# Optimization experiments

Hardware: AMD Instinct MI355X
Metric: run time of the kernel (lower is better)

The kernel has to match this reference:

```python
import jax, jax.numpy as jnp
import numpy as np

TEMPERATURE = 0.07
MASK_VALUE = -10000.0
EPS = 1e-12  # matches F.normalize eps


def setup_inputs() -> dict:
    key = jax.random.key(0)
    k1, k2 = jax.random.split(key)
    B, D = 8192, 512
    embeddings = jax.random.normal(k1, (B, D), dtype=jnp.float32)
    positive_mask = jax.random.randint(k2, (B, B), 0, 2).astype(bool)
    return {"embeddings": embeddings, "positive_mask": positive_mask}


def reference(embeddings, positive_mask):
    B = embeddings.shape[0]
    # L2 normalize rows (F.normalize with eps clamp)
    norm = jnp.maximum(jnp.linalg.norm(embeddings, axis=1, keepdims=True), EPS)
    e = embeddings / norm
    sim = jnp.matmul(e, e.T) / TEMPERATURE  # (B, B)
    eye = jnp.eye(B, dtype=bool)
    sim = jnp.where(eye, MASK_VALUE, sim)
    pos = positive_mask & ~eye
    counts = pos.sum(axis=1)  # (B,)
    pos_sum = jnp.sum(jnp.where(pos, sim, 0.0), axis=1)  # (B,)
    lse = jax.nn.logsumexp(sim, axis=1)  # (B,)
    pos_mean = pos_sum / jnp.maximum(counts, 1).astype(sim.dtype)
    # rows with positives: -mean(pos) + lse; rows without: just lse
    row_loss = jnp.where(counts > 0, lse - pos_mean, lse)
    return jnp.mean(row_loss)
```

## Files before the change

kernel.cpp:

```cpp
#include <hip/hip_runtime.h>
#include <hip/hip_bf16.h>

#define BN_ 8192
#define DK_ 512
#define TEMP_INV 14.2857142857142857f
#define LOG2E_ 1.44269504088896f
#define MAXOFF 15.0f

typedef __bf16 bf16x8 __attribute__((ext_vector_type(8)));
typedef float f32x4 __attribute__((ext_vector_type(4)));

__device__ inline unsigned short f2bf(float f) {
    unsigned u = __float_as_uint(f);
    return (unsigned short)((u + 0x7FFFu + ((u >> 16) & 1u)) >> 16);
}

__global__ __launch_bounds__(256) void norm_kernel(const float* __restrict__ emb,
                                                   unsigned short* __restrict__ ebf) {
    const int row  = blockIdx.x * 4 + (threadIdx.x >> 6);
    const int lane = threadIdx.x & 63;
    const float4* src = reinterpret_cast<const float4*>(emb + (size_t)row * DK_);
    float4 v0 = src[lane];
    float4 v1 = src[lane + 64];
    float ss = v0.x*v0.x + v0.y*v0.y + v0.z*v0.z + v0.w*v0.w
             + v1.x*v1.x + v1.y*v1.y + v1.z*v1.z + v1.w*v1.w;
#pragma unroll
    for (int off = 1; off < 64; off <<= 1) ss += __shfl_xor(ss, off, 64);
    const float scale = 1.0f / fmaxf(sqrtf(ss), 1e-12f);
    uint2 o0, o1;
    o0.x = (unsigned)f2bf(v0.x * scale) | ((unsigned)f2bf(v0.y * scale) << 16);
    o0.y = (unsigned)f2bf(v0.z * scale) | ((unsigned)f2bf(v0.w * scale) << 16);
    o1.x = (unsigned)f2bf(v1.x * scale) | ((unsigned)f2bf(v1.y * scale) << 16);
    o1.y = (unsigned)f2bf(v1.z * scale) | ((unsigned)f2bf(v1.w * scale) << 16);
    uint2* dst = reinterpret_cast<uint2*>(ebf + (size_t)row * DK_);
    dst[lane]      = o0;
    dst[lane + 64] = o1;
}

__global__ __launch_bounds__(256) void infonce_main(
    const unsigned short* __restrict__ ebf,
    const int* __restrict__ mask,
    float* __restrict__ se, float* __restrict__ ps, float* __restrict__ ct) {

    __shared__ unsigned short As[128 * 64];
    __shared__ unsigned short Bs[128 * 64];
    __shared__ unsigned char  pmB[128 * 16];
    __shared__ float red2[2][128];

    const int t    = threadIdx.x;
    const int lane = t & 63;
    const int wid  = t >> 6;
    const int wr   = wid >> 1;
    const int wc   = wid & 1;
    const int rb   = blockIdx.x;
    const int cb   = blockIdx.y;

    if (t < 128) { red2[0][t] = 0.f; red2[1][t] = 0.f; }

    f32x4 acc[4][4] = {};

    const int sr = t >> 3;
    const int sc = (t & 7) * 8;
    const size_t arow0 = (size_t)(rb * 128 + sr) * DK_ + sc;
    const size_t brow0 = (size_t)(cb * 128 + sr) * DK_ + sc;

    const int mr = t >> 4;
    const int mc = t & 15;
    const int* mbase = mask + (size_t)(rb * 128 + mr) * BN_ + cb * 128 + mc * 8;

    const int r16 = lane & 15;
    const int kg  = (lane >> 4) * 8;

#pragma unroll
    for (int kt = 0; kt < 8; ++kt) {
        const int k0 = kt * 64;
#pragma unroll
        for (int s = 0; s < 4; ++s) {
            __builtin_amdgcn_global_load_lds(
                (const __attribute__((address_space(1))) void*)(ebf + arow0 + (size_t)s * 32 * DK_ + k0),
                (__attribute__((address_space(3))) void*)(As + s * 2048 + t * 8),
                16, 0, 0);
        }
#pragma unroll
        for (int s = 0; s < 4; ++s) {
            __builtin_amdgcn_global_load_lds(
                (const __attribute__((address_space(1))) void*)(ebf + brow0 + (size_t)s * 32 * DK_ + k0),
                (__attribute__((address_space(3))) void*)(Bs + s * 2048 + t * 8),
                16, 0, 0);
        }
        const int4* mp = reinterpret_cast<const int4*>(mbase + (size_t)kt * 16 * BN_);
        const int4 mv0 = mp[0];
        const int4 mv1 = mp[1];

        __syncthreads();

        {
            unsigned by = (unsigned)(mv0.x != 0)        | ((unsigned)(mv0.y != 0) << 1)
                        | ((unsigned)(mv0.z != 0) << 2) | ((unsigned)(mv0.w != 0) << 3)
                        | ((unsigned)(mv1.x != 0) << 4) | ((unsigned)(mv1.y != 0) << 5)
                        | ((unsigned)(mv1.z != 0) << 6) | ((unsigned)(mv1.w != 0) << 7);
            pmB[(kt * 16 + mr) * 16 + mc] = (unsigned char)by;
        }

#pragma unroll
        for (int ks = 0; ks < 2; ++ks) {
            bf16x8 af[4], bfr[4];
#pragma unroll
            for (int fm = 0; fm < 4; ++fm)
                af[fm] = *reinterpret_cast<const bf16x8*>(As + (wr * 64 + fm * 16 + r16) * 64 + ks * 32 + kg);
#pragma unroll
            for (int fn = 0; fn < 4; ++fn)
                bfr[fn] = *reinterpret_cast<const bf16x8*>(Bs + (wc * 64 + fn * 16 + r16) * 64 + ks * 32 + kg);
#pragma unroll
            for (int fm = 0; fm < 4; ++fm)
#pragma unroll
                for (int fn = 0; fn < 4; ++fn)
                    acc[fm][fn] = __builtin_amdgcn_mfma_f32_16x16x32_bf16(bfr[fn], af[fm], acc[fm][fn], 0, 0, 0);
        }
        __syncthreads();
    }

    const float C1 = TEMP_INV * LOG2E_;
    const float C2 = -MAXOFF * LOG2E_;
    const bool  db  = (rb == cb);
    const int   gq4 = (lane >> 4) * 4;

#pragma unroll
    for (int fm = 0; fm < 4; ++fm) {
        const int li = wr * 64 + fm * 16 + (lane & 15);
        const uint4 rv = *reinterpret_cast<const uint4*>(pmB + li * 16);
        const unsigned w0 = wc ? rv.z : rv.x;
        const unsigned w1 = wc ? rv.w : rv.y;
        float lsep = 0.f, posp = 0.f;
#pragma unroll
        for (int fn = 0; fn < 4; ++fn) {
            const unsigned wsel = (fn < 2) ? w0 : w1;
#pragma unroll
            for (int rg = 0; rg < 4; ++rg) {
                const float a = acc[fm][fn][rg];
                const bool dg = db && (wr == wc) && (fm == fn) && ((lane & 15) == gq4 + rg);
                const float ex = dg ? 0.0f : exp2f(fmaf(a, C1, C2));
                lsep += ex;
                const bool p = (((wsel >> ((fn & 1) * 16 + gq4 + rg)) & 1u) != 0u) && !dg;
                posp += p ? a : 0.0f;
            }
        }
        lsep += __shfl_xor(lsep, 16, 64); lsep += __shfl_xor(lsep, 32, 64);
        posp += __shfl_xor(posp, 16, 64); posp += __shfl_xor(posp, 32, 64);
        if ((lane >> 4) == 0) {
            atomicAdd(&red2[0][li], lsep);
            atomicAdd(&red2[1][li], posp * TEMP_INV);
        }
    }
    __syncthreads();
    if (t < 128) {
        const uint4 rv = *reinterpret_cast<const uint4*>(pmB + t * 16);
        float cnt = (float)(__popc(rv.x) + __popc(rv.y) + __popc(rv.z) + __popc(rv.w));
        if (db) {
            const unsigned wsel = (t < 64) ? ((t < 32) ? rv.x : rv.y)
                                           : ((t < 96) ? rv.z : rv.w);
            cnt -= (float)((wsel >> (t & 31)) & 1u);
        }
        const int i = rb * 128 + t;
        atomicAdd(&se[i], red2[0][t]);
        atomicAdd(&ps[i], red2[1][t]);
        atomicAdd(&ct[i], cnt);
    }
}

__global__ __launch_bounds__(256) void finalize_kernel(const float* __restrict__ se,
                                                       const float* __restrict__ ps,
                                                       const float* __restrict__ ct,
                                                       float* __restrict__ out) {
    __shared__ float red[256];
    const int t = threadIdx.x;
    const int i = blockIdx.x * 256 + t;
    const float lse = logf(se[i]) + MAXOFF;
    red[t] = lse - ps[i] / fmaxf(ct[i], 1.0f);
    __syncthreads();
    for (int s = 128; s > 0; s >>= 1) {
        if (t < s) red[t] += red[t + s];
        __syncthreads();
    }
    if (t == 0) atomicAdd(out, red[0] * (1.0f / (float)BN_));
}

extern "C" void kernel_launch(void* const* d_in, const int* in_sizes, int n_in,
                              void* d_out, int out_size, void* d_ws, size_t ws_size,
                              hipStream_t stream) {
    const float* emb  = (const float*)d_in[0];
    const int*   mask = (const int*)d_in[1];
    float* out = (float*)d_out;

    char* ws = (char*)d_ws;
    unsigned short* ebf = (unsigned short*)ws;
    float* se = (float*)(ws + (size_t)8 * 1024 * 1024);
    float* ps = se + BN_;
    float* ct = ps + BN_;

    hipMemsetAsync(se, 0, (size_t)3 * BN_ * sizeof(float), stream);
    hipMemsetAsync(out, 0, sizeof(float), stream);
    norm_kernel<<<BN_ / 4, 256, 0, stream>>>(emb, ebf);
    infonce_main<<<dim3(64, 64), 256, 0, stream>>>(ebf, mask, se, ps, ct);
    finalize_kernel<<<BN_ / 256, 256, 0, stream>>>(se, ps, ct, out);
}
```

Before: 133.6 us.

## Exploit similarity symmetry by computing only upper-triangular tiles

Launches only the 2080 upper-triangular 128x128 tiles of the similarity matrix and maps a linear block id to (rb, cb). Each off-diagonal tile loads both its mask tile and the transposed mask tile. It then accumulates the row-wise and column-wise exp sums and positive sums, halving the GEMM and exp work. The cost is a heavier epilogue with extra shuffles and shared atomics, uneven per-block work, and more global atomics per block.

```diff
diff --git a/kernel.cpp b/kernel.cpp
--- a/kernel.cpp
+++ b/kernel.cpp
@@ -44,18 +44,26 @@
 
     __shared__ unsigned short As[128 * 64];
     __shared__ unsigned short Bs[128 * 64];
-    __shared__ unsigned char  pmB[128 * 16];
-    __shared__ float red2[2][128];
+    __shared__ unsigned char  pmB [128 * 16];
+    __shared__ unsigned char  pmBT[128 * 16];
+    __shared__ float redR[2][128];
+    __shared__ float redC[2][128];
 
     const int t    = threadIdx.x;
     const int lane = t & 63;
     const int wid  = t >> 6;
     const int wr   = wid >> 1;
     const int wc   = wid & 1;
-    const int rb   = blockIdx.x;
-    const int cb   = blockIdx.y;
-
-    if (t < 128) { red2[0][t] = 0.f; red2[1][t] = 0.f; }
+
+    const int bid = blockIdx.x;
+    int rb = (int)((129.0f - sqrtf(16641.0f - 8.0f * (float)bid)) * 0.5f);
+    while (64 * (rb + 1) - ((rb + 1) * rb) / 2 <= bid) ++rb;
+    while (64 * rb - (rb * (rb - 1)) / 2 > bid) --rb;
+    const int cb = rb + (bid - (64 * rb - (rb * (rb - 1)) / 2));
+    const bool offd = (rb != cb);
+    const bool db   = !offd;
+
+    if (t < 128) { redR[0][t] = 0.f; redR[1][t] = 0.f; redC[0][t] = 0.f; redC[1][t] = 0.f; }
 
     f32x4 acc[4][4] = {};
 
@@ -66,7 +74,8 @@
 
     const int mr = t >> 4;
     const int mc = t & 15;
-    const int* mbase = mask + (size_t)(rb * 128 + mr) * BN_ + cb * 128 + mc * 8;
+    const int* mbase  = mask + (size_t)(rb * 128 + mr) * BN_ + cb * 128 + mc * 8;
+    const int* mbaseT = mask + (size_t)(cb * 128 + mr) * BN_ + rb * 128 + mc * 8;
 
     const int r16 = lane & 15;
     const int kg  = (lane >> 4) * 8;
@@ -91,6 +100,12 @@
         const int4* mp = reinterpret_cast<const int4*>(mbase + (size_t)kt * 16 * BN_);
         const int4 mv0 = mp[0];
         const int4 mv1 = mp[1];
+        int4 tw0, tw1;
+        if (offd) {
+            const int4* tp = reinterpret_cast<const int4*>(mbaseT + (size_t)kt * 16 * BN_);
+            tw0 = tp[0];
+            tw1 = tp[1];
+        }
 
         __syncthreads();
 
@@ -100,6 +115,13 @@
                         | ((unsigned)(mv1.x != 0) << 4) | ((unsigned)(mv1.y != 0) << 5)
                         | ((unsigned)(mv1.z != 0) << 6) | ((unsigned)(mv1.w != 0) << 7);
             pmB[(kt * 16 + mr) * 16 + mc] = (unsigned char)by;
+            if (offd) {
+                unsigned byT = (unsigned)(tw0.x != 0)        | ((unsigned)(tw0.y != 0) << 1)
+                             | ((unsigned)(tw0.z != 0) << 2) | ((unsigned)(tw0.w != 0) << 3)
+                             | ((unsigned)(tw1.x != 0) << 4) | ((unsigned)(tw1.y != 0) << 5)
+                             | ((unsigned)(tw1.z != 0) << 6) | ((unsigned)(tw1.w != 0) << 7);
+                pmBT[(kt * 16 + mr) * 16 + mc] = (unsigned char)byT;
+            }
         }
 
 #pragma unroll
@@ -122,34 +144,65 @@
 
     const float C1 = TEMP_INV * LOG2E_;
     const float C2 = -MAXOFF * LOG2E_;
-    const bool  db  = (rb == cb);
-    const int   gq4 = (lane >> 4) * 4;
-
+    const int l15 = lane & 15;
+    const int g   = lane >> 4;
+    const int gq4 = g * 4;
+
+    uint2 rw[4];
 #pragma unroll
     for (int fm = 0; fm < 4; ++fm) {
-        const int li = wr * 64 + fm * 16 + (lane & 15);
-        const uint4 rv = *reinterpret_cast<const uint4*>(pmB + li * 16);
-        const unsigned w0 = wc ? rv.z : rv.x;
-        const unsigned w1 = wc ? rv.w : rv.y;
-        float lsep = 0.f, posp = 0.f;
-#pragma unroll
-        for (int fn = 0; fn < 4; ++fn) {
-            const unsigned wsel = (fn < 2) ? w0 : w1;
-#pragma unroll
-            for (int rg = 0; rg < 4; ++rg) {
+        const uint4 rv = *reinterpret_cast<const uint4*>(pmB + (wr * 64 + fm * 16 + l15) * 16);
+        rw[fm].x = wc ? rv.z : rv.x;
+        rw[fm].y = wc ? rv.w : rv.y;
+    }
+    float lseA[4] = {0.f, 0.f, 0.f, 0.f};
+    float posA[4] = {0.f, 0.f, 0.f, 0.f};
+
+#pragma unroll
+    for (int fn = 0; fn < 4; ++fn) {
+#pragma unroll
+        for (int rg = 0; rg < 4; ++rg) {
+            const int jl = wc * 64 + fn * 16 + gq4 + rg;
+            uint2 tv;
+            if (offd) tv = *reinterpret_cast<const uint2*>(pmBT + jl * 16 + wr * 8);
+            float colL = 0.f, colP = 0.f;
+#pragma unroll
+            for (int fm = 0; fm < 4; ++fm) {
                 const float a = acc[fm][fn][rg];
-                const bool dg = db && (wr == wc) && (fm == fn) && ((lane & 15) == gq4 + rg);
+                const bool dg = db && (wr == wc) && (fm == fn) && (l15 == gq4 + rg);
                 const float ex = dg ? 0.0f : exp2f(fmaf(a, C1, C2));
-                lsep += ex;
+                lseA[fm] += ex;
+                const unsigned wsel = (fn < 2) ? rw[fm].x : rw[fm].y;
                 const bool p = (((wsel >> ((fn & 1) * 16 + gq4 + rg)) & 1u) != 0u) && !dg;
-                posp += p ? a : 0.0f;
+                posA[fm] += p ? a : 0.0f;
+                if (offd) {
+                    colL += ex;
+                    const unsigned cw = (fm < 2) ? tv.x : tv.y;
+                    colP += ((cw >> ((fm & 1) * 16 + l15)) & 1u) ? a : 0.0f;
+                }
             }
-        }
-        lsep += __shfl_xor(lsep, 16, 64); lsep += __shfl_xor(lsep, 32, 64);
-        posp += __shfl_xor(posp, 16, 64); posp += __shfl_xor(posp, 32, 64);
-        if ((lane >> 4) == 0) {
-            atomicAdd(&red2[0][li], lsep);
-            atomicAdd(&red2[1][li], posp * TEMP_INV);
+            if (offd) {
+#pragma unroll
+                for (int off = 1; off < 16; off <<= 1) {
+                    colL += __shfl_xor(colL, off, 64);
+                    colP += __shfl_xor(colP, off, 64);
+                }
+                if (l15 == 0) {
+                    atomicAdd(&redC[0][jl], colL);
+                    atomicAdd(&redC[1][jl], colP * TEMP_INV);
+                }
+            }
+        }
+    }
+#pragma unroll
+    for (int fm = 0; fm < 4; ++fm) {
+        float L = lseA[fm], P = posA[fm];
+        L += __shfl_xor(L, 16, 64); L += __shfl_xor(L, 32, 64);
+        P += __shfl_xor(P, 16, 64); P += __shfl_xor(P, 32, 64);
+        if (g == 0) {
+            const int li = wr * 64 + fm * 16 + l15;
+            atomicAdd(&redR[0][li], L);
+            atomicAdd(&redR[1][li], P * TEMP_INV);
         }
     }
     __syncthreads();
@@ -162,9 +215,17 @@
             cnt -= (float)((wsel >> (t & 31)) & 1u);
         }
         const int i = rb * 128 + t;
-        atomicAdd(&se[i], red2[0][t]);
-        atomicAdd(&ps[i], red2[1][t]);
+        atomicAdd(&se[i], redR[0][t]);
+        atomicAdd(&ps[i], redR[1][t]);
         atomicAdd(&ct[i], cnt);
+    } else if (offd) {
+        const int r = t - 128;
+        const uint4 tvr = *reinterpret_cast<const uint4*>(pmBT + r * 16);
+        const float cnt = (float)(__popc(tvr.x) + __popc(tvr.y) + __popc(tvr.z) + __popc(tvr.w));
+        const int j = cb * 128 + r;
+        atomicAdd(&se[j], redC[0][r]);
+        atomicAdd(&ps[j], redC[1][r]);
+        atomicAdd(&ct[j], cnt);
     }
 }
 
@@ -201,6 +262,6 @@
     hipMemsetAsync(se, 0, (size_t)3 * BN_ * sizeof(float), stream);
     hipMemsetAsync(out, 0, sizeof(float), stream);
     norm_kernel<<<BN_ / 4, 256, 0, stream>>>(emb, ebf);
-    infonce_main<<<dim3(64, 64), 256, 0, stream>>>(ebf, mask, se, ps, ct);
+    infonce_main<<<2080, 256, 0, stream>>>(ebf, mask, se, ps, ct);
     finalize_kernel<<<BN_ / 256, 256, 0, stream>>>(se, ps, ct, out);
 }
```

Result: slower. 224.6 us (+68.1%).

## Double-buffer LDS tiles and prefetch mask rows two stages ahead

Applied to the files above, without the earlier changes.

The main GEMM kernel now keeps two LDS buffers for the A and B tiles. It issues the global-to-LDS loads for the next k-step before computing the current one, and loads mask values two k-steps ahead into registers. Explicit vmcnt waits and one barrier per iteration replace the two __syncthreads, so memory latency can overlap the MFMA work. In exchange it doubles the tile LDS footprint, adds a launch bound of 2 blocks per CU that may constrain registers, and relies on hand-counted vmcnt values for correctness.

```diff
diff --git a/kernel.cpp b/kernel.cpp
--- a/kernel.cpp
+++ b/kernel.cpp
@@ -37,13 +37,13 @@
     dst[lane + 64] = o1;
 }
 
-__global__ __launch_bounds__(256) void infonce_main(
+__global__ __launch_bounds__(256, 2) void infonce_main(
     const unsigned short* __restrict__ ebf,
     const int* __restrict__ mask,
     float* __restrict__ se, float* __restrict__ ps, float* __restrict__ ct) {
 
-    __shared__ unsigned short As[128 * 64];
-    __shared__ unsigned short Bs[128 * 64];
+    __shared__ unsigned short As[2][128 * 64];
+    __shared__ unsigned short Bs[2][128 * 64];
     __shared__ unsigned char  pmB[128 * 16];
     __shared__ float red2[2][128];
 
@@ -71,54 +71,81 @@
     const int r16 = lane & 15;
     const int kg  = (lane >> 4) * 8;
 
+#define STAGE(buf, kt)                                                                     \
+    {                                                                                      \
+        const int k0_ = (kt) * 64;                                                         \
+        _Pragma("unroll")                                                                  \
+        for (int s = 0; s < 4; ++s) {                                                      \
+            __builtin_amdgcn_global_load_lds(                                              \
+                (const __attribute__((address_space(1))) void*)(ebf + arow0 + (size_t)s * 32 * DK_ + k0_), \
+                (__attribute__((address_space(3))) void*)(&As[buf][0] + s * 2048 + t * 8), \
+                16, 0, 0);                                                                 \
+        }                                                                                  \
+        _Pragma("unroll")                                                                  \
+        for (int s = 0; s < 4; ++s) {                                                      \
+            __builtin_amdgcn_global_load_lds(                                              \
+                (const __attribute__((address_space(1))) void*)(ebf + brow0 + (size_t)s * 32 * DK_ + k0_), \
+                (__attribute__((address_space(3))) void*)(&Bs[buf][0] + s * 2048 + t * 8), \
+                16, 0, 0);                                                                 \
+        }                                                                                  \
+    }
+
+    int4 m0[2], m1[2];
+
+    STAGE(0, 0);
+    asm volatile("" ::: "memory");
+    { const int4* p = reinterpret_cast<const int4*>(mbase);                       m0[0] = p[0]; m1[0] = p[1]; }
+    asm volatile("" ::: "memory");
+    { const int4* p = reinterpret_cast<const int4*>(mbase + (size_t)16 * BN_);    m0[1] = p[0]; m1[1] = p[1]; }
+    asm volatile("" ::: "memory");
+
 #pragma unroll
     for (int kt = 0; kt < 8; ++kt) {
-        const int k0 = kt * 64;
-#pragma unroll
-        for (int s = 0; s < 4; ++s) {
-            __builtin_amdgcn_global_load_lds(
-                (const __attribute__((address_space(1))) void*)(ebf + arow0 + (size_t)s * 32 * DK_ + k0),
-                (__attribute__((address_space(3))) void*)(As + s * 2048 + t * 8),
-                16, 0, 0);
-        }
-#pragma unroll
-        for (int s = 0; s < 4; ++s) {
-            __builtin_amdgcn_global_load_lds(
-                (const __attribute__((address_space(1))) void*)(ebf + brow0 + (size_t)s * 32 * DK_ + k0),
-                (__attribute__((address_space(3))) void*)(Bs + s * 2048 + t * 8),
-                16, 0, 0);
-        }
-        const int4* mp = reinterpret_cast<const int4*>(mbase + (size_t)kt * 16 * BN_);
-        const int4 mv0 = mp[0];
-        const int4 mv1 = mp[1];
-
-        __syncthreads();
+        if (kt < 7) { asm volatile("s_waitcnt vmcnt(2)" ::: "memory"); }
+        else        { asm volatile("s_waitcnt vmcnt(0)" ::: "memory"); }
+        __builtin_amdgcn_s_barrier();
+        __builtin_amdgcn_sched_barrier(0);
 
         {
-            unsigned by = (unsigned)(mv0.x != 0)        | ((unsigned)(mv0.y != 0) << 1)
-                        | ((unsigned)(mv0.z != 0) << 2) | ((unsigned)(mv0.w != 0) << 3)
-                        | ((unsigned)(mv1.x != 0) << 4) | ((unsigned)(mv1.y != 0) << 5)
-                        | ((unsigned)(mv1.z != 0) << 6) | ((unsigned)(mv1.w != 0) << 7);
+            const int4 a = m0[kt & 1], b = m1[kt & 1];
+            unsigned by = (unsigned)(a.x != 0)        | ((unsigned)(a.y != 0) << 1)
+                        | ((unsigned)(a.z != 0) << 2) | ((unsigned)(a.w != 0) << 3)
+                        | ((unsigned)(b.x != 0) << 4) | ((unsigned)(b.y != 0) << 5)
+                        | ((unsigned)(b.z != 0) << 6) | ((unsigned)(b.w != 0) << 7);
             pmB[(kt * 16 + mr) * 16 + mc] = (unsigned char)by;
         }
-
+        if (kt < 7) {
+            STAGE((kt + 1) & 1, kt + 1);
+            asm volatile("" ::: "memory");
+            if (kt < 6) {
+                const int4* p = reinterpret_cast<const int4*>(mbase + (size_t)(kt + 2) * 16 * BN_);
+                m0[kt & 1] = p[0];
+                m1[kt & 1] = p[1];
+            }
+            asm volatile("" ::: "memory");
+        }
+        __builtin_amdgcn_sched_barrier(0);
+
+        const unsigned short* Ab = &As[kt & 1][0];
+        const unsigned short* Bb = &Bs[kt & 1][0];
 #pragma unroll
         for (int ks = 0; ks < 2; ++ks) {
             bf16x8 af[4], bfr[4];
 #pragma unroll
             for (int fm = 0; fm < 4; ++fm)
-                af[fm] = *reinterpret_cast<const bf16x8*>(As + (wr * 64 + fm * 16 + r16) * 64 + ks * 32 + kg);
+                af[fm] = *reinterpret_cast<const bf16x8*>(Ab + (wr * 64 + fm * 16 + r16) * 64 + ks * 32 + kg);
 #pragma unroll
             for (int fn = 0; fn < 4; ++fn)
-                bfr[fn] = *reinterpret_cast<const bf16x8*>(Bs + (wc * 64 + fn * 16 + r16) * 64 + ks * 32 + kg);
+                bfr[fn] = *reinterpret_cast<const bf16x8*>(Bb + (wc * 64 + fn * 16 + r16) * 64 + ks * 32 + kg);
 #pragma unroll
             for (int fm = 0; fm < 4; ++fm)
 #pragma unroll
                 for (int fn = 0; fn < 4; ++fn)
                     acc[fm][fn] = __builtin_amdgcn_mfma_f32_16x16x32_bf16(bfr[fn], af[fm], acc[fm][fn], 0, 0, 0);
         }
-        __syncthreads();
-    }
+    }
+#undef STAGE
+    __syncthreads();
 
     const float C1 = TEMP_INV * LOG2E_;
     const float C2 = -MAXOFF * LOG2E_;
```

Result: slower. 157.9 us (+18.1%).
